# Kernel tuning notes

Hardware: AMD Instinct MI355X
Metric: run time of the kernel (lower is better)

The kernel has to match this reference:

```python
import jax, jax.numpy as jnp
import numpy as np

N_NODES = 100000
N_EDGES = 3200000
C = 256
NEG_SLOPE = 0.2


def setup_inputs() -> dict:
    key = jax.random.key(0)
    k1, k2, k3, k4 = jax.random.split(key, 4)
    x = jax.random.normal(k1, (N_NODES, C), dtype=jnp.float32)
    # xavier_uniform on (2C, 1): bound = sqrt(6/(2C+1))
    bound = float(np.sqrt(6.0 / (2 * C + 1)))
    att = jax.random.uniform(k2, (2 * C, 1), dtype=jnp.float32, minval=-bound, maxval=bound)
    row = jax.random.randint(k3, (N_EDGES,), 0, N_NODES, dtype=jnp.int64)
    col = jax.random.randint(k4, (N_EDGES,), 0, N_NODES, dtype=jnp.int64)
    edge_index = jnp.stack([row, col], axis=0)
    return {"x": x, "att": att, "edge_index": edge_index}


def reference(x, att, edge_index):
    # Original: alpha = leaky_relu(cat([x[row], x[col]], -1) @ att)
    # Equivalent split form avoids materializing the [E, 2C] concat:
    # alpha_e = (x @ att[:C])[row] + (x @ att[C:])[col]
    row, col = edge_index[0], edge_index[1]
    n = x.shape[0]
    c = x.shape[1]
    s_src = (x @ att[:c]).squeeze(-1)  # (N,)
    s_dst = (x @ att[c:]).squeeze(-1)  # (N,)
    alpha = jax.nn.leaky_relu(s_src[row] + s_dst[col], negative_slope=NEG_SLOPE)  # (E,)
    # scatter_softmax over edges grouped by destination row id
    m = jax.ops.segment_max(alpha, row, num_segments=n)          # (N,)
    e = jnp.exp(alpha - m[row])                                   # (E,)
    denom = jax.ops.segment_sum(e, row, num_segments=n)          # (N,)
    out = e / denom[row]                                          # (E,)
    # torch code transposes [E,1] -> [1,E] before scatter_softmax; squeeze(-1) is a no-op
    return out[None, :]
```

## Files before the change

### kernel.cpp

```cpp
#include <hip/hip_runtime.h>

#define NN 100000
#define NE 3200000
#define CC 256
#define NEG_SLOPE 0.2f

#define SEG_S 32
#define SEG_P 8
#define PART_SZ 12500
#define SEG_BLOCK 1024
#define ESLICE (NE / SEG_S)

typedef __attribute__((ext_vector_type(8))) _Float16 half8;

__global__ __launch_bounds__(256) void node_scores_kernel(
    const float* __restrict__ x,
    const float* __restrict__ att,
    float* __restrict__ s_src,
    float* __restrict__ s_dst) {
  int gid  = blockIdx.x * blockDim.x + threadIdx.x;
  int node = gid >> 6;
  int lane = threadIdx.x & 63;
  if (node >= NN) return;
  const float4* xr = (const float4*)(x + (size_t)node * CC);
  const float4* a0 = (const float4*)att;
  const float4* a1 = (const float4*)(att + CC);
  float4 xv = xr[lane];
  float4 av = a0[lane];
  float4 bv = a1[lane];
  float s0 = xv.x * av.x + xv.y * av.y + xv.z * av.z + xv.w * av.w;
  float s1 = xv.x * bv.x + xv.y * bv.y + xv.z * bv.z + xv.w * bv.w;
#pragma unroll
  for (int off = 32; off > 0; off >>= 1) {
    s0 += __shfl_down(s0, off, 64);
    s1 += __shfl_down(s1, off, 64);
  }
  if (lane == 0) {
    s_src[node] = s0;
    s_dst[node] = s1;
  }
}

__global__ __launch_bounds__(256) void edge_exp_kernel(
    const int4* __restrict__ row4,
    const int4* __restrict__ col4,
    const float* __restrict__ s_src,
    const float* __restrict__ s_dst,
    half8* __restrict__ e_out) {
  int i = blockIdx.x * blockDim.x + threadIdx.x;
  if (i >= NE / 8) return;
  int4 ra = row4[2 * i], rb = row4[2 * i + 1];
  int4 ca = col4[2 * i], cb = col4[2 * i + 1];
  float a0 = s_src[ra.x] + s_dst[ca.x];
  float a1 = s_src[ra.y] + s_dst[ca.y];
  float a2 = s_src[ra.z] + s_dst[ca.z];
  float a3 = s_src[ra.w] + s_dst[ca.w];
  float a4 = s_src[rb.x] + s_dst[cb.x];
  float a5 = s_src[rb.y] + s_dst[cb.y];
  float a6 = s_src[rb.z] + s_dst[cb.z];
  float a7 = s_src[rb.w] + s_dst[cb.w];
  a0 = (a0 > 0.0f) ? a0 : NEG_SLOPE * a0;
  a1 = (a1 > 0.0f) ? a1 : NEG_SLOPE * a1;
  a2 = (a2 > 0.0f) ? a2 : NEG_SLOPE * a2;
  a3 = (a3 > 0.0f) ? a3 : NEG_SLOPE * a3;
  a4 = (a4 > 0.0f) ? a4 : NEG_SLOPE * a4;
  a5 = (a5 > 0.0f) ? a5 : NEG_SLOPE * a5;
  a6 = (a6 > 0.0f) ? a6 : NEG_SLOPE * a6;
  a7 = (a7 > 0.0f) ? a7 : NEG_SLOPE * a7;
  half8 h;
  h[0] = (_Float16)__expf(a0);
  h[1] = (_Float16)__expf(a1);
  h[2] = (_Float16)__expf(a2);
  h[3] = (_Float16)__expf(a3);
  h[4] = (_Float16)__expf(a4);
  h[5] = (_Float16)__expf(a5);
  h[6] = (_Float16)__expf(a6);
  h[7] = (_Float16)__expf(a7);
  e_out[i] = h;
}

__global__ __launch_bounds__(SEG_BLOCK) void segsum_kernel(
    const int* __restrict__ row,
    const _Float16* __restrict__ e,
    float* __restrict__ partial ) {
  __shared__ float lds[PART_SZ];
  int s = blockIdx.x;
  int p = blockIdx.y;
  for (int i = threadIdx.x; i < PART_SZ; i += SEG_BLOCK) lds[i] = 0.0f;
  __syncthreads();
  int lo = p * PART_SZ;
  const int4*  row4 = (const int4*)(row + s * ESLICE);
  const half8* e8   = (const half8*)(e + (size_t)s * ESLICE);
  const int n8 = ESLICE / 8;
  for (int i = threadIdx.x; i < n8; i += SEG_BLOCK) {
    int4 ra = row4[2 * i], rb = row4[2 * i + 1];
    half8 ev = e8[i];
    int r0 = ra.x - lo; if ((unsigned)r0 < PART_SZ) atomicAdd(&lds[r0], (float)ev[0]);
    int r1 = ra.y - lo; if ((unsigned)r1 < PART_SZ) atomicAdd(&lds[r1], (float)ev[1]);
    int r2 = ra.z - lo; if ((unsigned)r2 < PART_SZ) atomicAdd(&lds[r2], (float)ev[2]);
    int r3 = ra.w - lo; if ((unsigned)r3 < PART_SZ) atomicAdd(&lds[r3], (float)ev[3]);
    int r4 = rb.x - lo; if ((unsigned)r4 < PART_SZ) atomicAdd(&lds[r4], (float)ev[4]);
    int r5 = rb.y - lo; if ((unsigned)r5 < PART_SZ) atomicAdd(&lds[r5], (float)ev[5]);
    int r6 = rb.z - lo; if ((unsigned)r6 < PART_SZ) atomicAdd(&lds[r6], (float)ev[6]);
    int r7 = rb.w - lo; if ((unsigned)r7 < PART_SZ) atomicAdd(&lds[r7], (float)ev[7]);
  }
  __syncthreads();
  float* outp = partial + (size_t)s * NN + lo;
  for (int i = threadIdx.x; i < PART_SZ; i += SEG_BLOCK) outp[i] = lds[i];
}

__global__ __launch_bounds__(256) void reduce_kernel(
    const float* __restrict__ partial,
    float* __restrict__ denom) {
  int n4 = blockIdx.x * blockDim.x + threadIdx.x;
  if (n4 >= NN / 4) return;
  float4 sum = make_float4(0.f, 0.f, 0.f, 0.f);
#pragma unroll
  for (int s = 0; s < SEG_S; ++s) {
    float4 v = ((const float4*)(partial + (size_t)s * NN))[n4];
    sum.x += v.x; sum.y += v.y; sum.z += v.z; sum.w += v.w;
  }
  ((float4*)denom)[n4] = make_float4(1.f / sum.x, 1.f / sum.y, 1.f / sum.z, 1.f / sum.w);
}

__global__ __launch_bounds__(256) void edge_div_kernel(
    const int4* __restrict__ row4,
    const half8* __restrict__ e,
    const float* __restrict__ denom,
    float4* __restrict__ out4) {
  int i = blockIdx.x * blockDim.x + threadIdx.x;
  if (i >= NE / 8) return;
  int4 ra = row4[2 * i], rb = row4[2 * i + 1];
  half8 ev = e[i];
  float4 oa, ob;
  oa.x = (float)ev[0] * denom[ra.x];
  oa.y = (float)ev[1] * denom[ra.y];
  oa.z = (float)ev[2] * denom[ra.z];
  oa.w = (float)ev[3] * denom[ra.w];
  ob.x = (float)ev[4] * denom[rb.x];
  ob.y = (float)ev[5] * denom[rb.y];
  ob.z = (float)ev[6] * denom[rb.z];
  ob.w = (float)ev[7] * denom[rb.w];
  out4[2 * i]     = oa;
  out4[2 * i + 1] = ob;
}

extern "C" void kernel_launch(void* const* d_in, const int* in_sizes, int n_in,
                              void* d_out, int out_size, void* d_ws, size_t ws_size,
                              hipStream_t stream) {
  const float* x   = (const float*)d_in[0];
  const float* att = (const float*)d_in[1];
  const int* ei    = (const int*)d_in[2];
  const int* row   = ei;
  const int4* row4 = (const int4*)ei;
  const int4* col4 = (const int4*)(ei + NE);
  float4* out4     = (float4*)d_out;

  float* s_src      = (float*)d_ws;
  float* s_dst      = s_src + NN;
  float* denom      = s_dst + NN;
  _Float16* e_buf   = (_Float16*)(denom + NN);
  float* partial    = (float*)(e_buf + NE);

  node_scores_kernel<<<(NN * 64 + 255) / 256, 256, 0, stream>>>(x, att, s_src, s_dst);
  edge_exp_kernel<<<(NE / 8 + 255) / 256, 256, 0, stream>>>(
      row4, col4, s_src, s_dst, (half8*)e_buf);
  dim3 seg_grid(SEG_S, SEG_P);
  segsum_kernel<<<seg_grid, SEG_BLOCK, 0, stream>>>(row, e_buf, partial);
  reduce_kernel<<<(NN / 4 + 255) / 256, 256, 0, stream>>>(partial, denom);
  edge_div_kernel<<<(NE / 8 + 255) / 256, 256, 0, stream>>>(
      row4, (const half8*)e_buf, denom, out4);
}
```

Baseline: 234.8 us.

## Fuse segment sum into edge exp kernel via global atomics into replicated partials

Removes the separate LDS-partitioned segsum kernel and instead performs global float atomicAdds into one of 8 replicated partial arrays directly inside the edge exp kernel, with a zero kernel and a smaller reduce. This avoids re-reading row indices and e values and the 8x redundant scanning of the old partitioned segsum. The node score kernel is also changed to use 16 lanes per node with a shorter xor reduction. The cost is 3.2M random global atomics, which may contend or be slow relative to LDS atomics.

```diff
diff --git a/kernel.cpp b/kernel.cpp
--- a/kernel.cpp
+++ b/kernel.cpp
@@ -4,38 +4,42 @@
 #define NE 3200000
 #define CC 256
 #define NEG_SLOPE 0.2f
-
-#define SEG_S 32
-#define SEG_P 8
-#define PART_SZ 12500
-#define SEG_BLOCK 1024
-#define ESLICE (NE / SEG_S)
+#define NCOPY 8
 
 typedef __attribute__((ext_vector_type(8))) _Float16 half8;
+
+__global__ __launch_bounds__(256) void zero_kernel(float4* __restrict__ p, int n4) {
+  int i = blockIdx.x * blockDim.x + threadIdx.x;
+  if (i < n4) p[i] = make_float4(0.f, 0.f, 0.f, 0.f);
+}
 
 __global__ __launch_bounds__(256) void node_scores_kernel(
     const float* __restrict__ x,
     const float* __restrict__ att,
     float* __restrict__ s_src,
     float* __restrict__ s_dst) {
-  int gid  = blockIdx.x * blockDim.x + threadIdx.x;
-  int node = gid >> 6;
-  int lane = threadIdx.x & 63;
+  int t   = blockIdx.x * blockDim.x + threadIdx.x;
+  int node = t >> 4;
+  int gl   = t & 15;
   if (node >= NN) return;
-  const float4* xr = (const float4*)(x + (size_t)node * CC);
-  const float4* a0 = (const float4*)att;
-  const float4* a1 = (const float4*)(att + CC);
-  float4 xv = xr[lane];
-  float4 av = a0[lane];
-  float4 bv = a1[lane];
-  float s0 = xv.x * av.x + xv.y * av.y + xv.z * av.z + xv.w * av.w;
-  float s1 = xv.x * bv.x + xv.y * bv.y + xv.z * bv.z + xv.w * bv.w;
+  const float4* xr = (const float4*)(x + (size_t)node * CC) + gl * 4;
+  const float4* a0 = (const float4*)att + gl * 4;
+  const float4* a1 = (const float4*)(att + CC) + gl * 4;
+  float s0 = 0.f, s1 = 0.f;
 #pragma unroll
-  for (int off = 32; off > 0; off >>= 1) {
-    s0 += __shfl_down(s0, off, 64);
-    s1 += __shfl_down(s1, off, 64);
+  for (int j = 0; j < 4; ++j) {
+    float4 xv = xr[j];
+    float4 av = a0[j];
+    float4 bv = a1[j];
+    s0 += xv.x * av.x + xv.y * av.y + xv.z * av.z + xv.w * av.w;
+    s1 += xv.x * bv.x + xv.y * bv.y + xv.z * bv.z + xv.w * bv.w;
   }
-  if (lane == 0) {
+#pragma unroll
+  for (int m = 8; m >= 1; m >>= 1) {
+    s0 += __shfl_xor(s0, m, 64);
+    s1 += __shfl_xor(s1, m, 64);
+  }
+  if (gl == 0) {
     s_src[node] = s0;
     s_dst[node] = s1;
   }
@@ -46,9 +50,11 @@
     const int4* __restrict__ col4,
     const float* __restrict__ s_src,
     const float* __restrict__ s_dst,
-    half8* __restrict__ e_out) {
+    half8* __restrict__ e_out,
+    float* __restrict__ partial ) {
   int i = blockIdx.x * blockDim.x + threadIdx.x;
   if (i >= NE / 8) return;
+  float* part = partial + (size_t)(blockIdx.x & (NCOPY - 1)) * NN;
   int4 ra = row4[2 * i], rb = row4[2 * i + 1];
   int4 ca = col4[2 * i], cb = col4[2 * i + 1];
   float a0 = s_src[ra.x] + s_dst[ca.x];
@@ -77,50 +83,25 @@
   h[6] = (_Float16)__expf(a6);
   h[7] = (_Float16)__expf(a7);
   e_out[i] = h;
-}
-
-__global__ __launch_bounds__(SEG_BLOCK) void segsum_kernel(
-    const int* __restrict__ row,
-    const _Float16* __restrict__ e,
-    float* __restrict__ partial ) {
-  __shared__ float lds[PART_SZ];
-  int s = blockIdx.x;
-  int p = blockIdx.y;
-  for (int i = threadIdx.x; i < PART_SZ; i += SEG_BLOCK) lds[i] = 0.0f;
-  __syncthreads();
-  int lo = p * PART_SZ;
-  const int4*  row4 = (const int4*)(row + s * ESLICE);
-  const half8* e8   = (const half8*)(e + (size_t)s * ESLICE);
-  const int n8 = ESLICE / 8;
-  for (int i = threadIdx.x; i < n8; i += SEG_BLOCK) {
-    int4 ra = row4[2 * i], rb = row4[2 * i + 1];
-    half8 ev = e8[i];
-    int r0 = ra.x - lo; if ((unsigned)r0 < PART_SZ) atomicAdd(&lds[r0], (float)ev[0]);
-    int r1 = ra.y - lo; if ((unsigned)r1 < PART_SZ) atomicAdd(&lds[r1], (float)ev[1]);
-    int r2 = ra.z - lo; if ((unsigned)r2 < PART_SZ) atomicAdd(&lds[r2], (float)ev[2]);
-    int r3 = ra.w - lo; if ((unsigned)r3 < PART_SZ) atomicAdd(&lds[r3], (float)ev[3]);
-    int r4 = rb.x - lo; if ((unsigned)r4 < PART_SZ) atomicAdd(&lds[r4], (float)ev[4]);
-    int r5 = rb.y - lo; if ((unsigned)r5 < PART_SZ) atomicAdd(&lds[r5], (float)ev[5]);
-    int r6 = rb.z - lo; if ((unsigned)r6 < PART_SZ) atomicAdd(&lds[r6], (float)ev[6]);
-    int r7 = rb.w - lo; if ((unsigned)r7 < PART_SZ) atomicAdd(&lds[r7], (float)ev[7]);
-  }
-  __syncthreads();
-  float* outp = partial + (size_t)s * NN + lo;
-  for (int i = threadIdx.x; i < PART_SZ; i += SEG_BLOCK) outp[i] = lds[i];
+  atomicAdd(&part[ra.x], (float)h[0]);
+  atomicAdd(&part[ra.y], (float)h[1]);
+  atomicAdd(&part[ra.z], (float)h[2]);
+  atomicAdd(&part[ra.w], (float)h[3]);
+  atomicAdd(&part[rb.x], (float)h[4]);
+  atomicAdd(&part[rb.y], (float)h[5]);
+  atomicAdd(&part[rb.z], (float)h[6]);
+  atomicAdd(&part[rb.w], (float)h[7]);
 }
 
 __global__ __launch_bounds__(256) void reduce_kernel(
     const float* __restrict__ partial,
     float* __restrict__ denom) {
-  int n4 = blockIdx.x * blockDim.x + threadIdx.x;
-  if (n4 >= NN / 4) return;
-  float4 sum = make_float4(0.f, 0.f, 0.f, 0.f);
+  int n = blockIdx.x * blockDim.x + threadIdx.x;
+  if (n >= NN) return;
+  float s = 0.f;
 #pragma unroll
-  for (int s = 0; s < SEG_S; ++s) {
-    float4 v = ((const float4*)(partial + (size_t)s * NN))[n4];
-    sum.x += v.x; sum.y += v.y; sum.z += v.z; sum.w += v.w;
-  }
-  ((float4*)denom)[n4] = make_float4(1.f / sum.x, 1.f / sum.y, 1.f / sum.z, 1.f / sum.w);
+  for (int c = 0; c < NCOPY; ++c) s += partial[(size_t)c * NN + n];
+  denom[n] = 1.f / s;
 }
 
 __global__ __launch_bounds__(256) void edge_div_kernel(
@@ -151,23 +132,22 @@
   const float* x   = (const float*)d_in[0];
   const float* att = (const float*)d_in[1];
   const int* ei    = (const int*)d_in[2];
-  const int* row   = ei;
   const int4* row4 = (const int4*)ei;
   const int4* col4 = (const int4*)(ei + NE);
   float4* out4     = (float4*)d_out;
 
-  float* s_src      = (float*)d_ws;
-  float* s_dst      = s_src + NN;
-  float* denom      = s_dst + NN;
-  _Float16* e_buf   = (_Float16*)(denom + NN);
-  float* partial    = (float*)(e_buf + NE);
+  float* s_src    = (float*)d_ws;
+  float* s_dst    = s_src + NN;
+  float* denom    = s_dst + NN;
+  _Float16* e_buf = (_Float16*)(denom + NN);
+  float* partial  = (float*)(e_buf + NE);
 
-  node_scores_kernel<<<(NN * 64 + 255) / 256, 256, 0, stream>>>(x, att, s_src, s_dst);
+  zero_kernel<<<(NCOPY * NN / 4 + 255) / 256, 256, 0, stream>>>(
+      (float4*)partial, NCOPY * NN / 4);
+  node_scores_kernel<<<(NN * 16 + 255) / 256, 256, 0, stream>>>(x, att, s_src, s_dst);
   edge_exp_kernel<<<(NE / 8 + 255) / 256, 256, 0, stream>>>(
-      row4, col4, s_src, s_dst, (half8*)e_buf);
-  dim3 seg_grid(SEG_S, SEG_P);
-  segsum_kernel<<<seg_grid, SEG_BLOCK, 0, stream>>>(row, e_buf, partial);
-  reduce_kernel<<<(NN / 4 + 255) / 256, 256, 0, stream>>>(partial, denom);
+      row4, col4, s_src, s_dst, (half8*)e_buf, partial);
+  reduce_kernel<<<(NN + 255) / 256, 256, 0, stream>>>(partial, denom);
   edge_div_kernel<<<(NE / 8 + 255) / 256, 256, 0, stream>>>(
       row4, (const half8*)e_buf, denom, out4);
 }
```

New measurement: 349.5 us. 1.49x slower.
